# Kernel optimization log

Hardware: AMD Instinct MI355X
Metric: run time of the kernel (lower is better)

The kernel has to match this reference:

```python
import jax, jax.numpy as jnp
import numpy as np

N = 2048          # n_nodes
D = 512           # d_model
H = 8             # n_heads
DH = D // H       # head dim
FF = 4 * D
MAX_DIST = 10
LN_EPS = 1e-5


def setup_inputs() -> dict:
    key = jax.random.key(0)
    ks = jax.random.split(key, 20)
    s = 1.0 / np.sqrt(D)
    sf = 1.0 / np.sqrt(FF)
    return {
        "x": jax.random.normal(ks[0], (N, D), jnp.float32),
        "adj": (jax.random.uniform(ks[1], (N, N)) < 0.01).astype(jnp.float32),
        "spatial_emb": jax.random.normal(ks[2], (MAX_DIST + 1,), jnp.float32) * 0.02,
        "wq": jax.random.normal(ks[3], (D, D), jnp.float32) * s,
        "bq": jnp.zeros((D,), jnp.float32),
        "wk": jax.random.normal(ks[4], (D, D), jnp.float32) * s,
        "bk": jnp.zeros((D,), jnp.float32),
        "wv": jax.random.normal(ks[5], (D, D), jnp.float32) * s,
        "bv": jnp.zeros((D,), jnp.float32),
        "wo": jax.random.normal(ks[6], (D, D), jnp.float32) * s,
        "bo": jnp.zeros((D,), jnp.float32),
        "ln1_w": jnp.ones((D,), jnp.float32),
        "ln1_b": jnp.zeros((D,), jnp.float32),
        "w1": jax.random.normal(ks[7], (FF, D), jnp.float32) * s,
        "b1": jnp.zeros((FF,), jnp.float32),
        "w2": jax.random.normal(ks[8], (D, FF), jnp.float32) * sf,
        "b2": jnp.zeros((D,), jnp.float32),
        "ln2_w": jnp.ones((D,), jnp.float32),
        "ln2_b": jnp.zeros((D,), jnp.float32),
    }


def floyd_warshall(adj):
    # dist init: 1 where edge, inf otherwise, 0 on diagonal
    n = adj.shape[0]
    dist = jnp.where(adj > 0, 1.0, jnp.inf)
    dist = jnp.where(jnp.eye(n, dtype=bool), 0.0, dist)

    def body(k, dmat):
        row = jax.lax.dynamic_slice_in_dim(dmat, k, 1, axis=0)  # [1, n]
        col = jax.lax.dynamic_slice_in_dim(dmat, k, 1, axis=1)  # [n, 1]
        return jnp.minimum(dmat, col + row)

    dist = jax.lax.fori_loop(0, n, body, dist)
    return jnp.clip(dist, 0, MAX_DIST).astype(jnp.int32)  # [n, n]


def layer_norm(x, w, b):
    mu = jnp.mean(x, axis=-1, keepdims=True)
    var = jnp.mean(jnp.square(x - mu), axis=-1, keepdims=True)
    return (x - mu) * jax.lax.rsqrt(var + LN_EPS) * w + b


def reference(x, adj, spatial_emb, wq, bq, wk, bk, wv, bv, wo, bo,
              ln1_w, ln1_b, w1, b1, w2, b2, ln2_w, ln2_b):
    n = x.shape[0]
    sp_dist = floyd_warshall(adj)                       # [n, n] int32 in [0, 10]
    bias = spatial_emb[sp_dist]                         # [n, n] additive attn bias

    # multi-head attention with additive spatial bias (shared across heads)
    q = (x @ wq.T + bq).reshape(n, H, DH).transpose(1, 0, 2)  # [h, n, dh]
    k = (x @ wk.T + bk).reshape(n, H, DH).transpose(1, 0, 2)
    v = (x @ wv.T + bv).reshape(n, H, DH).transpose(1, 0, 2)
    scores = jnp.einsum('hnd,hmd->hnm', q, k) / np.sqrt(DH) + bias[None]
    attn = jax.nn.softmax(scores, axis=-1)
    ctx = jnp.einsum('hnm,hmd->hnd', attn, v)           # [h, n, dh]
    attn_out = ctx.transpose(1, 0, 2).reshape(n, D) @ wo.T + bo

    h = layer_norm(x + attn_out, ln1_w, ln1_b)
    ffn = jax.nn.gelu(h @ w1.T + b1, approximate=False) @ w2.T + b2
    return layer_norm(h + ffn, ln2_w, ln2_b)
```

## Files before the change

### kernel.cpp

```cpp
#include <hip/hip_runtime.h>
#include <cstdint>
#include <cstddef>


typedef __attribute__((ext_vector_type(8))) short short8;
typedef __attribute__((ext_vector_type(4))) float f32x4;

#define N_NODES 2048
#define DMODEL  512
#define NHEAD   8
#define DHEAD   64
#define FFDIM   2048

#define OFF_ADJB   (0)
#define OFF_DIST   (0x80000)
#define OFF_XB     (0x480000)
#define OFF_WQB    (0x680000)
#define OFF_WKB    (0x700000)
#define OFF_WVB    (0x780000)
#define OFF_WOB    (0x800000)
#define OFF_W1B    (0x880000)
#define OFF_W2B    (0xA80000)
#define OFF_QM     (0xC80000)
#define OFF_KM     (0xE80000)
#define OFF_VT     (0x1080000)
#define OFF_CTX    (0x1280000)
#define OFF_ATMP   (0x1480000)
#define OFF_H1     (0x1880000)
#define OFF_H1B    (0x1C80000)
#define OFF_MID    (0x1E80000)
#define OFF_FFN2   (0x2680000)

__device__ __forceinline__ unsigned short f2bf(float f) {
  union { float f; unsigned u; } c; c.f = f;
  unsigned r = c.u + 0x7FFFu + ((c.u >> 16) & 1u);
  return (unsigned short)(r >> 16);
}

__device__ __forceinline__ float bf2f(unsigned short u) {
  union { unsigned u; float f; } c; c.u = ((unsigned)u) << 16;
  return c.f;
}

__device__ __forceinline__ uint32_t cvtpk_bf16(float lo, float hi) {
  uint32_t r;
  asm("v_cvt_pk_bf16_f32 %0, %1, %2" : "=v"(r) : "v"(lo), "v"(hi));
  return r;
}

typedef const __attribute__((address_space(1))) unsigned int* as1_u32p;
typedef __attribute__((address_space(3))) unsigned int* as3_u32p;
__device__ __forceinline__ void gload_lds16(const void* g, void* l) {
  __builtin_amdgcn_global_load_lds((as1_u32p)g, (as3_u32p)l, 16, 0, 0);
}

__global__ void cvt_all_kernel(const float* __restrict__ x,
                               const float* __restrict__ wq, const float* __restrict__ wk,
                               const float* __restrict__ wv, const float* __restrict__ wo,
                               const float* __restrict__ w1, const float* __restrict__ w2,
                               unsigned short* __restrict__ xb,
                               unsigned short* __restrict__ wqb, unsigned short* __restrict__ wkb,
                               unsigned short* __restrict__ wvb, unsigned short* __restrict__ wob,
                               unsigned short* __restrict__ w1b, unsigned short* __restrict__ w2b) {
  int i = blockIdx.x * 256 + threadIdx.x;
  const float* src; unsigned short* dst; int off;
  if (i < 262144)      { src = x;  dst = xb;  off = i; }
  else if (i < 327680) { src = wq; dst = wqb; off = i - 262144; }
  else if (i < 393216) { src = wk; dst = wkb; off = i - 327680; }
  else if (i < 458752) { src = wv; dst = wvb; off = i - 393216; }
  else if (i < 524288) { src = wo; dst = wob; off = i - 458752; }
  else if (i < 786432) { src = w1; dst = w1b; off = i - 524288; }
  else                 { src = w2; dst = w2b; off = i - 786432; }
  float4 v = ((const float4*)src)[off];
  unsigned p0 = (unsigned)f2bf(v.x) | ((unsigned)f2bf(v.y) << 16);
  unsigned p1 = (unsigned)f2bf(v.z) | ((unsigned)f2bf(v.w) << 16);
  ((uint2*)dst)[off] = make_uint2(p0, p1);
}

__global__ void pack_adj_kernel(const float* __restrict__ adj, uint32_t* __restrict__ adjb) {
  int i = blockIdx.x;
  int tid = threadIdx.x, wid = tid >> 6, lane = tid & 63;
  for (int it = 0; it < 8; ++it) {
    int jbase = it * 256 + wid * 64;
    int j = jbase + lane;
    unsigned long long m = __ballot(adj[(size_t)i * 2048 + j] > 0.0f);
    int w32 = jbase >> 5;
    if (lane == 0)  adjb[i * 64 + w32]     = (uint32_t)m;
    if (lane == 32) adjb[i * 64 + w32 + 1] = (uint32_t)(m >> 32);
  }
}

__global__ __launch_bounds__(256) void bfs_kernel(const uint32_t* __restrict__ adjb,
                                                  uint8_t* __restrict__ dist) {
  int i = blockIdx.x;
  int tid = threadIdx.x, wid = tid >> 6, lane = tid & 63;

  __shared__ uint16_t list_s[2112];
  __shared__ uint4 comb_v[4][64];
  __shared__ uint32_t wtot[4];
  const uint32_t* comb_u = (const uint32_t*)comb_v;

  uint32_t adjrow = adjb[i * 64 + lane];
  uint32_t diagm  = (lane == (i >> 5)) ? (1u << (i & 31)) : 0u;
  uint32_t front  = adjrow & ~diagm;
  uint32_t reach  = front | diagm;
  uint32_t dp0 = front;
  uint32_t dp1 = ~(front | diagm);
  uint32_t dp2 = 0u;
  uint32_t dp3 = dp1;

  for (int t = 2; t <= 9; ++t) {
    uint32_t fw = __shfl(front, wid * 16 + (lane >> 2));
    uint32_t fb = (fw >> ((lane & 3) * 8)) & 0xFFu;
    int cnt = __popc(fb);
    int scan = cnt;
    #pragma unroll
    for (int o = 1; o < 64; o <<= 1) {
      int u = __shfl_up(scan, o);
      if (lane >= o) scan += u;
    }
    if (lane == 63) wtot[wid] = (uint32_t)scan;
    __syncthreads();
    int w0 = (int)wtot[0], w1 = (int)wtot[1], w2 = (int)wtot[2], w3 = (int)wtot[3];
    int cnt_total = w0 + w1 + w2 + w3;
    if (cnt_total == 0) break;
    int base0 = (wid > 0 ? w0 : 0) + (wid > 1 ? w1 : 0) + (wid > 2 ? w2 : 0);
    int off = base0 + scan - cnt;
    int nodebase = tid * 8;
    while (fb) {
      int b = __builtin_ctz(fb);
      fb &= fb - 1u;
      list_s[off++] = (uint16_t)(nodebase + b);
    }
    int padded = (cnt_total + 63) & ~63;
    for (int k = cnt_total + tid; k < padded; k += 256)
      list_s[k] = (uint16_t)i;
    __syncthreads();

    uint4 acc = make_uint4(0u, 0u, 0u, 0u);
    int wsub = (lane & 15) * 4;
    for (int base = wid * 16; base < padded; base += 64) {
      #pragma unroll
      for (int j = 0; j < 4; ++j) {
        int node = list_s[base + j * 4 + (lane >> 4)];
        uint4 v = *(const uint4*)(adjb + node * 64 + wsub);
        acc.x |= v.x; acc.y |= v.y; acc.z |= v.z; acc.w |= v.w;
      }
    }
    comb_v[wid][lane] = acc;
    __syncthreads();
    uint32_t orv = 0;
    int idx = (lane >> 2) * 4 + (lane & 3);
    #pragma unroll
    for (int w4 = 0; w4 < 4; ++w4)
      #pragma unroll
      for (int g = 0; g < 4; ++g)
        orv |= comb_u[w4 * 256 + g * 64 + idx];
    uint32_t nreach = reach | orv;
    uint32_t nf = nreach & ~reach;
    dp0 = (dp0 & ~nf) | ((t & 1) ? nf : 0u);
    dp1 = (dp1 & ~nf) | ((t & 2) ? nf : 0u);
    dp2 = (dp2 & ~nf) | ((t & 4) ? nf : 0u);
    dp3 = (dp3 & ~nf) | ((t & 8) ? nf : 0u);
    front = nf;
    reach = nreach;
    __syncthreads();
  }

  uint32_t p0 = __shfl(dp0, wid * 16 + (lane >> 2));
  uint32_t p1 = __shfl(dp1, wid * 16 + (lane >> 2));
  uint32_t p2 = __shfl(dp2, wid * 16 + (lane >> 2));
  uint32_t p3 = __shfl(dp3, wid * 16 + (lane >> 2));
  int sh = (lane & 3) * 8;
  uint32_t lo = 0, hi = 0;
  #pragma unroll
  for (int j = 0; j < 4; ++j) {
    int bit = sh + j;
    uint32_t d = ((p0 >> bit) & 1u) | (((p1 >> bit) & 1u) << 1) |
                 (((p2 >> bit) & 1u) << 2) | (((p3 >> bit) & 1u) << 3);
    lo |= d << (8 * j);
  }
  #pragma unroll
  for (int j = 0; j < 4; ++j) {
    int bit = sh + 4 + j;
    uint32_t d = ((p0 >> bit) & 1u) | (((p1 >> bit) & 1u) << 1) |
                 (((p2 >> bit) & 1u) << 2) | (((p3 >> bit) & 1u) << 3);
    hi |= d << (8 * j);
  }
  ((uint2*)(dist + (size_t)i * 2048))[tid] = make_uint2(lo, hi);
}

__device__ __forceinline__ void gemm_core64(const short* __restrict__ A,
                                            const short* __restrict__ W,
                                            int K, int kstart, int kc,
                                            int am0, int bn0,
                                            f32x4 acc[2][2], char* smem) {
  int tid = threadIdx.x, wid = tid >> 6, lane = tid & 63;
  int c15 = lane & 15, g = lane >> 4;
  int wm = wid >> 1, wn = wid & 1;
  char* As = smem;
  char* Bs = smem + 8192;

  for (int kt = kstart; kt < kstart + kc; kt += 64) {
    __syncthreads();
    #pragma unroll
    for (int i = 0; i < 2; ++i) {
      int c   = i * 256 + tid;
      int row = c >> 3;
      int kg  = (c & 7) ^ (row & 7);
      gload_lds16(A + (size_t)(am0 + row) * K + kt + kg * 8,
                  As + i * 4096 + wid * 1024);
      gload_lds16(W + (size_t)(bn0 + row) * K + kt + kg * 8,
                  Bs + i * 4096 + wid * 1024);
    }
    __syncthreads();
    #pragma unroll
    for (int ks = 0; ks < 2; ++ks) {
      short8 af[2], bfr[2];
      #pragma unroll
      for (int mt = 0; mt < 2; ++mt) {
        int row   = wm * 32 + mt * 16 + c15;
        int chunk = (ks * 4 + g) ^ (row & 7);
        af[mt] = *(const short8*)(As + row * 128 + chunk * 16);
      }
      #pragma unroll
      for (int nt = 0; nt < 2; ++nt) {
        int row   = wn * 32 + nt * 16 + c15;
        int chunk = (ks * 4 + g) ^ (row & 7);
        bfr[nt] = *(const short8*)(Bs + row * 128 + chunk * 16);
      }
      #pragma unroll
      for (int mt = 0; mt < 2; ++mt)
        #pragma unroll
        for (int nt = 0; nt < 2; ++nt)
          acc[mt][nt] = __builtin_amdgcn_mfma_f32_16x16x32_bf16(af[mt], bfr[nt], acc[mt][nt], 0, 0, 0);
    }
  }
}

template <int MODE>
__global__ __launch_bounds__(256) void gemm_kernel(
    const short* __restrict__ A,
    const short* __restrict__ W0, const short* __restrict__ W1, const short* __restrict__ W2,
    const float* __restrict__ b0, const float* __restrict__ b1, const float* __restrict__ b2,
    unsigned short* __restrict__ outq, unsigned short* __restrict__ outk, unsigned short* __restrict__ outv,
    float* __restrict__ of0, float* __restrict__ of1, float* __restrict__ of2, float* __restrict__ of3,
    unsigned short* __restrict__ outb,
    int K, int kc, int ldo) {
  __shared__ __align__(16) char smem[16384];
  int by = blockIdx.y, z = blockIdx.z;
  const short* W; const float* bias; int bn0;
  int region = 0;
  if (MODE == 0) {
    region = by >> 3;
    W    = (region == 0) ? W0 : (region == 1) ? W1 : W2;
    bias = (region == 0) ? b0 : (region == 1) ? b1 : b2;
    bn0  = (by & 7) * 64;
  } else {
    W = W0; bias = b0; bn0 = by * 64;
  }
  int am0 = blockIdx.x * 64;

  f32x4 acc[2][2] = {};
  gemm_core64(A, W, K, z * kc, kc, am0, bn0, acc, smem);

  int tid = threadIdx.x, wid = tid >> 6, lane = tid & 63;
  int c15 = lane & 15, g = lane >> 4;
  int wm = wid >> 1, wn = wid & 1;
  float* of = (MODE == 1) ? ((z == 0) ? of0 : (z == 1) ? of1 : (z == 2) ? of2 : of3) : of0;

  #pragma unroll
  for (int mt = 0; mt < 2; ++mt)
    #pragma unroll
    for (int nt = 0; nt < 2; ++nt)
      #pragma unroll
      for (int r = 0; r < 4; ++r) {
        int row = am0 + wm * 32 + mt * 16 + g * 4 + r;
        int col = bn0 + wn * 32 + nt * 16 + c15;
        if (MODE == 0) {
          float v = acc[mt][nt][r] + bias[col];
          if (region == 0)      outq[(size_t)row * 512 + col] = f2bf(v);
          else if (region == 1) outk[(size_t)row * 512 + col] = f2bf(v);
          else                  outv[(size_t)col * 2048 + row] = f2bf(v);
        } else if (MODE == 1) {
          float v = acc[mt][nt][r] + ((z == 0) ? bias[col] : 0.0f);
          of[(size_t)row * ldo + col] = v;
        } else {
          float v = acc[mt][nt][r] + bias[col];
          float gv = 0.5f * v * (1.0f + erff(v * 0.70710678118654752f));
          outb[(size_t)row * ldo + col] = f2bf(gv);
        }
      }
}

__global__ __launch_bounds__(256, 4) void attn_kernel(
    const short* __restrict__ qm, const short* __restrict__ km,
    const short* __restrict__ vT, const uint8_t* __restrict__ dist,
    const float* __restrict__ semb, unsigned short* __restrict__ po,
    float* __restrict__ pml) {
  int qt = blockIdx.x, h = blockIdx.y, z = blockIdx.z;
  int tid = threadIdx.x, wid = tid >> 6, lane = tid & 63;
  int c15 = lane & 15, g = lane >> 4;

  __shared__ __align__(16) char Ks[8192];
  __shared__ __align__(16) char Vs[8192];
  __shared__ __align__(16) uint8_t Ds[4096];
  __shared__ float semb_s[12];
  if (tid < 11) semb_s[tid] = semb[tid];

  int q0  = qt * 64;
  int wq0 = q0 + wid * 16;
  int kvz = z * 512;

  short8 aq[2];
  #pragma unroll
  for (int ks = 0; ks < 2; ++ks)
    aq[ks] = *(const short8*)(qm + (size_t)(wq0 + c15) * 512 + h * 64 + ks * 32 + g * 8);

  int i  = tid;
  int r0 = i >> 3,        c0 = (i & 7) ^ (r0 & 7);
  int r1 = (256 + i) >> 3, c1 = ((256 + i) & 7) ^ (r1 & 7);
  int dr = i >> 2,        dc = (i & 3) ^ (dr & 3);

  f32x4 o[4] = {};
  float m = -1e30f, l = 0.0f;

  for (int t = 0; t < 8; ++t) {
    int kv0 = kvz + t * 64;

    __syncthreads();
    gload_lds16(km + (size_t)(kv0 + r0) * 512 + h * 64 + c0 * 8, Ks + wid * 1024);
    gload_lds16(km + (size_t)(kv0 + r1) * 512 + h * 64 + c1 * 8, Ks + 4096 + wid * 1024);
    gload_lds16(vT + (size_t)(h * 64 + r0) * 2048 + kv0 + c0 * 8, Vs + wid * 1024);
    gload_lds16(vT + (size_t)(h * 64 + r1) * 2048 + kv0 + c1 * 8, Vs + 4096 + wid * 1024);
    gload_lds16(dist + (size_t)(q0 + dr) * 2048 + kv0 + dc * 16, Ds + wid * 1024);
    __syncthreads();

    f32x4 sacc[4] = {};
    __builtin_amdgcn_s_setprio(1);
    #pragma unroll
    for (int nt = 0; nt < 4; ++nt) {
      int row = nt * 16 + c15;
      #pragma unroll
      for (int ks = 0; ks < 2; ++ks) {
        short8 bk = *(const short8*)(Ks + row * 128 + (((ks * 4 + g) ^ (row & 7)) * 16));
        sacc[nt] = __builtin_amdgcn_mfma_f32_16x16x32_bf16(bk, aq[ks], sacc[nt], 0, 0, 0);
      }
    }
    __builtin_amdgcn_s_setprio(0);

    int drow = wid * 16 + c15;
    float rmax = -1e30f;
    #pragma unroll
    for (int nt = 0; nt < 4; ++nt) {
      uint32_t d32 = *(const uint32_t*)(Ds + drow * 64 + ((nt ^ (drow & 3)) * 16) + g * 4);
      #pragma unroll
      for (int r = 0; r < 4; ++r) {
        float s = sacc[nt][r] * 0.125f + semb_s[(d32 >> (8 * r)) & 0xFFu];
        sacc[nt][r] = s;
        rmax = fmaxf(rmax, s);
      }
    }
    rmax = fmaxf(rmax, __shfl_xor(rmax, 16));
    rmax = fmaxf(rmax, __shfl_xor(rmax, 32));

    float mn = fmaxf(m, rmax);
    float pscale = __expf(m - mn);
    m = mn;
    float rsum = 0.0f;
    #pragma unroll
    for (int nt = 0; nt < 4; ++nt)
      #pragma unroll
      for (int r = 0; r < 4; ++r) {
        float p = __expf(sacc[nt][r] - m);
        sacc[nt][r] = p;
        rsum += p;
      }
    rsum += __shfl_xor(rsum, 16);
    rsum += __shfl_xor(rsum, 32);
    l = l * pscale + rsum;

    float psr[4];
    #pragma unroll
    for (int r = 0; r < 4; ++r) psr[r] = __shfl(pscale, g * 4 + r);
    #pragma unroll
    for (int dt = 0; dt < 4; ++dt)
      #pragma unroll
      for (int r = 0; r < 4; ++r)
        o[dt][r] *= psr[r];

    int src_lo = c15 + (g & 1) * 32;
    int src_hi = src_lo + 16;
    int sel = g >> 1;
    short8 pa[2];
    {
      uint32_t p00 = cvtpk_bf16(sacc[0][0], sacc[0][1]);
      uint32_t p01 = cvtpk_bf16(sacc[0][2], sacc[0][3]);
      uint32_t p10 = cvtpk_bf16(sacc[1][0], sacc[1][1]);
      uint32_t p11 = cvtpk_bf16(sacc[1][2], sacc[1][3]);
      uint32_t a0 = (uint32_t)__shfl((int)p00, src_lo);
      uint32_t a1 = (uint32_t)__shfl((int)p01, src_lo);
      uint32_t a2 = (uint32_t)__shfl((int)p00, src_hi);
      uint32_t a3 = (uint32_t)__shfl((int)p01, src_hi);
      uint32_t b0 = (uint32_t)__shfl((int)p10, src_lo);
      uint32_t b1 = (uint32_t)__shfl((int)p11, src_lo);
      uint32_t b2 = (uint32_t)__shfl((int)p10, src_hi);
      uint32_t b3 = (uint32_t)__shfl((int)p11, src_hi);
      union { short8 s8; uint32_t u[4]; } up;
      up.u[0] = sel ? b0 : a0;
      up.u[1] = sel ? b1 : a1;
      up.u[2] = sel ? b2 : a2;
      up.u[3] = sel ? b3 : a3;
      pa[0] = up.s8;
    }
    {
      uint32_t p00 = cvtpk_bf16(sacc[2][0], sacc[2][1]);
      uint32_t p01 = cvtpk_bf16(sacc[2][2], sacc[2][3]);
      uint32_t p10 = cvtpk_bf16(sacc[3][0], sacc[3][1]);
      uint32_t p11 = cvtpk_bf16(sacc[3][2], sacc[3][3]);
      uint32_t a0 = (uint32_t)__shfl((int)p00, src_lo);
      uint32_t a1 = (uint32_t)__shfl((int)p01, src_lo);
      uint32_t a2 = (uint32_t)__shfl((int)p00, src_hi);
      uint32_t a3 = (uint32_t)__shfl((int)p01, src_hi);
      uint32_t b0 = (uint32_t)__shfl((int)p10, src_lo);
      uint32_t b1 = (uint32_t)__shfl((int)p11, src_lo);
      uint32_t b2 = (uint32_t)__shfl((int)p10, src_hi);
      uint32_t b3 = (uint32_t)__shfl((int)p11, src_hi);
      union { short8 s8; uint32_t u[4]; } up;
      up.u[0] = sel ? b0 : a0;
      up.u[1] = sel ? b1 : a1;
      up.u[2] = sel ? b2 : a2;
      up.u[3] = sel ? b3 : a3;
      pa[1] = up.s8;
    }

    __builtin_amdgcn_s_setprio(1);
    #pragma unroll
    for (int dt = 0; dt < 4; ++dt) {
      int row = dt * 16 + c15;
      #pragma unroll
      for (int ks = 0; ks < 2; ++ks) {
        short8 bv = *(const short8*)(Vs + row * 128 + (((ks * 4 + g) ^ (row & 7)) * 16));
        o[dt] = __builtin_amdgcn_mfma_f32_16x16x32_bf16(pa[ks], bv, o[dt], 0, 0, 0);
      }
    }
    __builtin_amdgcn_s_setprio(0);
  }

  #pragma unroll
  for (int dt = 0; dt < 4; ++dt)
    #pragma unroll
    for (int r = 0; r < 4; ++r) {
      int q = wq0 + g * 4 + r;
      po[((size_t)z * 2048 + q) * 512 + h * 64 + dt * 16 + c15] = f2bf(o[dt][r]);
    }
  if (g == 0) {
    int q = wq0 + c15;
    pml[(((size_t)z * 2048 + q) * 8 + h) * 2]     = m;
    pml[(((size_t)z * 2048 + q) * 8 + h) * 2 + 1] = l;
  }
}

__global__ __launch_bounds__(256) void attn_combine_kernel(
    const unsigned short* __restrict__ po, const float* __restrict__ pml,
    unsigned short* __restrict__ ctx) {
  int q = blockIdx.x, tid = threadIdx.x;
  #pragma unroll
  for (int half = 0; half < 2; ++half) {
    int d = half * 256 + tid;
    int h = d >> 6;
    float mm[4], ll[4];
    float ms = -1e30f;
    #pragma unroll
    for (int zz = 0; zz < 4; ++zz) {
      mm[zz] = pml[(((size_t)zz * 2048 + q) * 8 + h) * 2];
      ll[zz] = pml[(((size_t)zz * 2048 + q) * 8 + h) * 2 + 1];
      ms = fmaxf(ms, mm[zz]);
    }
    float num = 0.0f, den = 0.0f;
    #pragma unroll
    for (int zz = 0; zz < 4; ++zz) {
      float e = __expf(mm[zz] - ms);
      num += bf2f(po[((size_t)zz * 2048 + q) * 512 + d]) * e;
      den += ll[zz] * e;
    }
    ctx[(size_t)q * 512 + d] = f2bf(num / den);
  }
}

template <int NP, bool WB>
__global__ __launch_bounds__(256) void ln_kernel(
    const float* __restrict__ a,
    const float* __restrict__ p0, const float* __restrict__ p1,
    const float* __restrict__ p2, const float* __restrict__ p3,
    const float* __restrict__ w, const float* __restrict__ bb,
    float* __restrict__ out, unsigned short* __restrict__ outb) {
  int row = blockIdx.x, tid = threadIdx.x;
  size_t base = (size_t)row * 512;
  float v0 = a[base + tid]       + p0[base + tid];
  float v1 = a[base + tid + 256] + p0[base + tid + 256];
  if (NP > 1) { v0 += p1[base + tid]; v1 += p1[base + tid + 256]; }
  if (NP > 2) { v0 += p2[base + tid]; v1 += p2[base + tid + 256]; }
  if (NP > 3) { v0 += p3[base + tid]; v1 += p3[base + tid + 256]; }
  float s = v0 + v1, q = v0 * v0 + v1 * v1;
  for (int o = 32; o > 0; o >>= 1) { s += __shfl_down(s, o); q += __shfl_down(q, o); }
  __shared__ float rs[4], rq[4], bc[2];
  int wid = tid >> 6, lane = tid & 63;
  if (lane == 0) { rs[wid] = s; rq[wid] = q; }
  __syncthreads();
  if (tid == 0) {
    float S = rs[0] + rs[1] + rs[2] + rs[3];
    float Q = rq[0] + rq[1] + rq[2] + rq[3];
    float mu = S * (1.0f / 512.0f);
    bc[0] = mu;
    bc[1] = Q * (1.0f / 512.0f) - mu * mu;
  }
  __syncthreads();
  float mu = bc[0], inv = rsqrtf(bc[1] + 1e-5f);
  float o0 = (v0 - mu) * inv * w[tid] + bb[tid];
  float o1 = (v1 - mu) * inv * w[tid + 256] + bb[tid + 256];
  out[base + tid] = o0;
  out[base + tid + 256] = o1;
  if (WB) {
    outb[base + tid] = f2bf(o0);
    outb[base + tid + 256] = f2bf(o1);
  }
}

extern "C" void kernel_launch(void* const* d_in, const int* in_sizes, int n_in,
                              void* d_out, int out_size, void* d_ws, size_t ws_size,
                              hipStream_t stream) {
  (void)in_sizes; (void)n_in; (void)out_size; (void)ws_size;
  const float* x    = (const float*)d_in[0];
  const float* adj  = (const float*)d_in[1];
  const float* semb = (const float*)d_in[2];
  const float* wq   = (const float*)d_in[3];
  const float* bq   = (const float*)d_in[4];
  const float* wk   = (const float*)d_in[5];
  const float* bk   = (const float*)d_in[6];
  const float* wv   = (const float*)d_in[7];
  const float* bv   = (const float*)d_in[8];
  const float* wo   = (const float*)d_in[9];
  const float* bo   = (const float*)d_in[10];
  const float* ln1w = (const float*)d_in[11];
  const float* ln1b = (const float*)d_in[12];
  const float* w1   = (const float*)d_in[13];
  const float* b1   = (const float*)d_in[14];
  const float* w2   = (const float*)d_in[15];
  const float* b2   = (const float*)d_in[16];
  const float* ln2w = (const float*)d_in[17];
  const float* ln2b = (const float*)d_in[18];
  float* out = (float*)d_out;
  char* ws = (char*)d_ws;

  uint32_t*       adjb = (uint32_t*)(ws + OFF_ADJB);
  uint8_t*        dist = (uint8_t*)(ws + OFF_DIST);
  unsigned short* xb   = (unsigned short*)(ws + OFF_XB);
  unsigned short* wqb  = (unsigned short*)(ws + OFF_WQB);
  unsigned short* wkb  = (unsigned short*)(ws + OFF_WKB);
  unsigned short* wvb  = (unsigned short*)(ws + OFF_WVB);
  unsigned short* wob  = (unsigned short*)(ws + OFF_WOB);
  unsigned short* w1b  = (unsigned short*)(ws + OFF_W1B);
  unsigned short* w2b  = (unsigned short*)(ws + OFF_W2B);
  unsigned short* qm   = (unsigned short*)(ws + OFF_QM);
  unsigned short* km   = (unsigned short*)(ws + OFF_KM);
  unsigned short* vT   = (unsigned short*)(ws + OFF_VT);
  unsigned short* ctx  = (unsigned short*)(ws + OFF_CTX);
  float*          atmp = (float*)(ws + OFF_ATMP);
  float*          h1   = (float*)(ws + OFF_H1);
  unsigned short* h1b  = (unsigned short*)(ws + OFF_H1B);
  unsigned short* mid  = (unsigned short*)(ws + OFF_MID);
  float*          ffn2 = (float*)(ws + OFF_FFN2);
  unsigned short* po   = (unsigned short*)(ws + OFF_MID);
  float* pml   = (float*)(ws + OFF_FFN2);
  float* distf = (float*)(ws + OFF_DIST);
  float* qmf   = (float*)(ws + OFF_QM);
  float* vtf   = (float*)(ws + OFF_VT);

  cvt_all_kernel<<<4096, 256, 0, stream>>>(x, wq, wk, wv, wo, w1, w2,
                                           xb, wqb, wkb, wvb, wob, w1b, w2b);

  pack_adj_kernel<<<2048, 256, 0, stream>>>(adj, adjb);
  bfs_kernel<<<2048, 256, 0, stream>>>(adjb, dist);

  gemm_kernel<0><<<dim3(32, 24), 256, 0, stream>>>(
      (const short*)xb, (const short*)wqb, (const short*)wkb, (const short*)wvb,
      bq, bk, bv, qm, km, vT,
      nullptr, nullptr, nullptr, nullptr, nullptr, 512, 512, 512);

  attn_kernel<<<dim3(32, 8, 4), 256, 0, stream>>>(
      (const short*)qm, (const short*)km, (const short*)vT, dist, semb, po, pml);
  attn_combine_kernel<<<2048, 256, 0, stream>>>(po, pml, ctx);

  gemm_kernel<1><<<dim3(32, 8, 2), 256, 0, stream>>>(
      (const short*)ctx, (const short*)wob, nullptr, nullptr,
      bo, nullptr, nullptr, nullptr, nullptr, nullptr,
      atmp, distf, nullptr, nullptr, nullptr, 512, 256, 512);

  ln_kernel<2, true><<<2048, 256, 0, stream>>>(x, atmp, distf, nullptr, nullptr,
                                               ln1w, ln1b, h1, h1b);

  gemm_kernel<2><<<dim3(32, 32), 256, 0, stream>>>(
      (const short*)h1b, (const short*)w1b, nullptr, nullptr,
      b1, nullptr, nullptr, nullptr, nullptr, nullptr,
      nullptr, nullptr, nullptr, nullptr, mid, 512, 512, 2048);

  gemm_kernel<1><<<dim3(32, 8, 4), 256, 0, stream>>>(
      (const short*)mid, (const short*)w2b, nullptr, nullptr,
      b2, nullptr, nullptr, nullptr, nullptr, nullptr,
      ffn2, distf, qmf, vtf, nullptr, 2048, 512, 512);

  ln_kernel<4, false><<<2048, 256, 0, stream>>>(h1, ffn2, distf, qmf, vtf,
                                                ln2w, ln2b, out, nullptr);
}
```

Measured before the change: 141.4 us.

## Merge BFS and QKV projection into one launch to run concurrently

The BFS distance kernel and the QKV projection GEMM are independent, so they are fused into a single launch. Blocks below 2048 run BFS rows and the remaining 768 blocks compute QKV tiles, sharing one 16KB shared-memory buffer. This removes a kernel launch and lets the small GEMM fill the GPU alongside BFS rather than running after it. In exchange, the fused kernel's occupancy is set by the larger register and LDS footprint of the two bodies. The QKV mode is removed from the generic gemm template.

```diff
diff --git a/kernel.cpp b/kernel.cpp
--- a/kernel.cpp
+++ b/kernel.cpp
@@ -90,14 +90,13 @@
   }
 }
 
-__global__ __launch_bounds__(256) void bfs_kernel(const uint32_t* __restrict__ adjb,
-                                                  uint8_t* __restrict__ dist) {
-  int i = blockIdx.x;
+__device__ __forceinline__ void bfs_body(int i, const uint32_t* __restrict__ adjb,
+                                         uint8_t* __restrict__ dist, char* smem) {
   int tid = threadIdx.x, wid = tid >> 6, lane = tid & 63;
 
-  __shared__ uint16_t list_s[2112];
-  __shared__ uint4 comb_v[4][64];
-  __shared__ uint32_t wtot[4];
+  uint4* comb_v = (uint4*)smem;
+  uint32_t* wtot = (uint32_t*)(smem + 4096);
+  uint16_t* list_s = (uint16_t*)(smem + 4112);
   const uint32_t* comb_u = (const uint32_t*)comb_v;
 
   uint32_t adjrow = adjb[i * 64 + lane];
@@ -147,7 +146,7 @@
         acc.x |= v.x; acc.y |= v.y; acc.z |= v.z; acc.w |= v.w;
       }
     }
-    comb_v[wid][lane] = acc;
+    comb_v[wid * 64 + lane] = acc;
     __syncthreads();
     uint32_t orv = 0;
     int idx = (lane >> 2) * 4 + (lane & 3);
@@ -238,36 +237,78 @@
   }
 }
 
+__device__ __forceinline__ void qkv_body(int bx, int by,
+    const short* __restrict__ A,
+    const short* __restrict__ W0, const short* __restrict__ W1, const short* __restrict__ W2,
+    const float* __restrict__ b0, const float* __restrict__ b1, const float* __restrict__ b2,
+    unsigned short* __restrict__ outq, unsigned short* __restrict__ outk,
+    unsigned short* __restrict__ outv, char* smem) {
+  int region = by >> 3;
+  const short* W    = (region == 0) ? W0 : (region == 1) ? W1 : W2;
+  const float* bias = (region == 0) ? b0 : (region == 1) ? b1 : b2;
+  int bn0 = (by & 7) * 64;
+  int am0 = bx * 64;
+
+  f32x4 acc[2][2] = {};
+  gemm_core64(A, W, 512, 0, 512, am0, bn0, acc, smem);
+
+  int tid = threadIdx.x, wid = tid >> 6, lane = tid & 63;
+  int c15 = lane & 15, g = lane >> 4;
+  int wm = wid >> 1, wn = wid & 1;
+
+  #pragma unroll
+  for (int mt = 0; mt < 2; ++mt)
+    #pragma unroll
+    for (int nt = 0; nt < 2; ++nt)
+      #pragma unroll
+      for (int r = 0; r < 4; ++r) {
+        int row = am0 + wm * 32 + mt * 16 + g * 4 + r;
+        int col = bn0 + wn * 32 + nt * 16 + c15;
+        float v = acc[mt][nt][r] + bias[col];
+        if (region == 0)      outq[(size_t)row * 512 + col] = f2bf(v);
+        else if (region == 1) outk[(size_t)row * 512 + col] = f2bf(v);
+        else                  outv[(size_t)col * 2048 + row] = f2bf(v);
+      }
+}
+
+__global__ __launch_bounds__(256) void bfs_qkv_kernel(
+    const uint32_t* __restrict__ adjb, uint8_t* __restrict__ dist,
+    const short* __restrict__ xb,
+    const short* __restrict__ wqb, const short* __restrict__ wkb, const short* __restrict__ wvb,
+    const float* __restrict__ bq, const float* __restrict__ bk, const float* __restrict__ bv,
+    unsigned short* __restrict__ qm, unsigned short* __restrict__ km,
+    unsigned short* __restrict__ vT) {
+  __shared__ __align__(16) char smem[16384];
+  int b = blockIdx.x;
+  if (b < 2048) {
+    bfs_body(b, adjb, dist, smem);
+  } else {
+    int gidx = b - 2048;
+    qkv_body(gidx & 31, gidx >> 5, xb, wqb, wkb, wvb, bq, bk, bv, qm, km, vT, smem);
+  }
+}
+
 template <int MODE>
 __global__ __launch_bounds__(256) void gemm_kernel(
     const short* __restrict__ A,
-    const short* __restrict__ W0, const short* __restrict__ W1, const short* __restrict__ W2,
-    const float* __restrict__ b0, const float* __restrict__ b1, const float* __restrict__ b2,
-    unsigned short* __restrict__ outq, unsigned short* __restrict__ outk, unsigned short* __restrict__ outv,
-    float* __restrict__ of0, float* __restrict__ of1, float* __restrict__ of2, float* __restrict__ of3,
+    const short* __restrict__ W0,
+    const float* __restrict__ b0,
+    float* __restrict__ of0, float* __restrict__ of1,
+    float* __restrict__ of2, float* __restrict__ of3,
     unsigned short* __restrict__ outb,
     int K, int kc, int ldo) {
   __shared__ __align__(16) char smem[16384];
   int by = blockIdx.y, z = blockIdx.z;
-  const short* W; const float* bias; int bn0;
-  int region = 0;
-  if (MODE == 0) {
-    region = by >> 3;
-    W    = (region == 0) ? W0 : (region == 1) ? W1 : W2;
-    bias = (region == 0) ? b0 : (region == 1) ? b1 : b2;
-    bn0  = (by & 7) * 64;
-  } else {
-    W = W0; bias = b0; bn0 = by * 64;
-  }
+  int bn0 = by * 64;
   int am0 = blockIdx.x * 64;
 
   f32x4 acc[2][2] = {};
-  gemm_core64(A, W, K, z * kc, kc, am0, bn0, acc, smem);
+  gemm_core64(A, W0, K, z * kc, kc, am0, bn0, acc, smem);
 
   int tid = threadIdx.x, wid = tid >> 6, lane = tid & 63;
   int c15 = lane & 15, g = lane >> 4;
   int wm = wid >> 1, wn = wid & 1;
-  float* of = (MODE == 1) ? ((z == 0) ? of0 : (z == 1) ? of1 : (z == 2) ? of2 : of3) : of0;
+  float* of = (z == 0) ? of0 : (z == 1) ? of1 : (z == 2) ? of2 : of3;
 
   #pragma unroll
   for (int mt = 0; mt < 2; ++mt)
@@ -277,16 +318,11 @@
       for (int r = 0; r < 4; ++r) {
         int row = am0 + wm * 32 + mt * 16 + g * 4 + r;
         int col = bn0 + wn * 32 + nt * 16 + c15;
-        if (MODE == 0) {
-          float v = acc[mt][nt][r] + bias[col];
-          if (region == 0)      outq[(size_t)row * 512 + col] = f2bf(v);
-          else if (region == 1) outk[(size_t)row * 512 + col] = f2bf(v);
-          else                  outv[(size_t)col * 2048 + row] = f2bf(v);
-        } else if (MODE == 1) {
-          float v = acc[mt][nt][r] + ((z == 0) ? bias[col] : 0.0f);
+        if (MODE == 1) {
+          float v = acc[mt][nt][r] + ((z == 0) ? b0[col] : 0.0f);
           of[(size_t)row * ldo + col] = v;
         } else {
-          float v = acc[mt][nt][r] + bias[col];
+          float v = acc[mt][nt][r] + b0[col];
           float gv = 0.5f * v * (1.0f + erff(v * 0.70710678118654752f));
           outb[(size_t)row * ldo + col] = f2bf(gv);
         }
@@ -581,33 +617,29 @@
                                            xb, wqb, wkb, wvb, wob, w1b, w2b);
 
   pack_adj_kernel<<<2048, 256, 0, stream>>>(adj, adjb);
-  bfs_kernel<<<2048, 256, 0, stream>>>(adjb, dist);
-
-  gemm_kernel<0><<<dim3(32, 24), 256, 0, stream>>>(
-      (const short*)xb, (const short*)wqb, (const short*)wkb, (const short*)wvb,
-      bq, bk, bv, qm, km, vT,
-      nullptr, nullptr, nullptr, nullptr, nullptr, 512, 512, 512);
+
+  bfs_qkv_kernel<<<2816, 256, 0, stream>>>(
+      adjb, dist, (const short*)xb,
+      (const short*)wqb, (const short*)wkb, (const short*)wvb,
+      bq, bk, bv, qm, km, vT);
 
   attn_kernel<<<dim3(32, 8, 4), 256, 0, stream>>>(
       (const short*)qm, (const short*)km, (const short*)vT, dist, semb, po, pml);
   attn_combine_kernel<<<2048, 256, 0, stream>>>(po, pml, ctx);
 
   gemm_kernel<1><<<dim3(32, 8, 2), 256, 0, stream>>>(
-      (const short*)ctx, (const short*)wob, nullptr, nullptr,
-      bo, nullptr, nullptr, nullptr, nullptr, nullptr,
+      (const short*)ctx, (const short*)wob, bo,
       atmp, distf, nullptr, nullptr, nullptr, 512, 256, 512);
 
   ln_kernel<2, true><<<2048, 256, 0, stream>>>(x, atmp, distf, nullptr, nullptr,
                                                ln1w, ln1b, h1, h1b);
 
   gemm_kernel<2><<<dim3(32, 32), 256, 0, stream>>>(
-      (const short*)h1b, (const short*)w1b, nullptr, nullptr,
-      b1, nullptr, nullptr, nullptr, nullptr, nullptr,
+      (const short*)h1b, (const short*)w1b, b1,
       nullptr, nullptr, nullptr, nullptr, mid, 512, 512, 2048);
 
   gemm_kernel<1><<<dim3(32, 8, 4), 256, 0, stream>>>(
-      (const short*)mid, (const short*)w2b, nullptr, nullptr,
-      b2, nullptr, nullptr, nullptr, nullptr, nullptr,
+      (const short*)mid, (const short*)w2b, b2,
       ffn2, distf, qmf, vtf, nullptr, 2048, 512, 512);
 
   ln_kernel<4, false><<<2048, 256, 0, stream>>>(h1, ffn2, distf, qmf, vtf,
```

After: 142.0 us. About the same (+0.4%).
